# Kernel tuning notes

Hardware: AMD Instinct MI355X
Metric: run time of the kernel (lower is better)

The kernel has to match this reference:

```python
import jax, jax.numpy as jnp
import numpy as np

N, E = 50000, 800000
F_IN, C_PRE, C, G_HID = 16, 32, 64, 64
EPS = 1e-5


def graph_norm(x, batch, w, b, ms):
    # PyG GraphNorm over a single graph (batch all zeros)
    cnt = jax.ops.segment_sum(jnp.ones((x.shape[0], 1), x.dtype), batch, num_segments=1)
    mean = jax.ops.segment_sum(x, batch, num_segments=1) / cnt
    out = x - mean[batch] * ms
    var = jax.ops.segment_sum(out * out, batch, num_segments=1) / cnt
    std = jnp.sqrt(var + EPS)
    return w * out / std[batch] + b


def ggnn_conv(h, edge_index, edge_attr,
              gw1, gb1, gw2, gb2, gw3, gb3,
              zw, zb, rw, rb, hw, hb):
    n = h.shape[0]
    loops = jnp.arange(n)
    row = jnp.concatenate([edge_index[0], loops])  # sources (x_j)
    col = jnp.concatenate([edge_index[1], loops])  # targets (x_i), aggregation index
    ea = jnp.concatenate([edge_attr, jnp.ones((n, 1), h.dtype)], axis=0)
    deg = jax.ops.segment_sum(jnp.ones(col.shape[0], h.dtype), col, num_segments=n)
    dis = jnp.where(deg > 0, deg ** -0.5, 0.0)
    norm = dis[row] * dis[col]
    x_j = h[row]
    x_i = h[col]
    g = jnp.concatenate([x_i, x_j, ea], axis=-1)            # [E+N, 2C+1]
    g = jax.nn.relu(g @ gw1 + gb1)
    g = jax.nn.relu(g @ gw2 + gb2)
    gate = jax.nn.sigmoid(g @ gw3 + gb3)                     # [E+N, 1]
    msg = gate * (norm[:, None] * x_j)
    aggr = jax.ops.segment_sum(msg, col, num_segments=n)     # scatter-add
    zi = jnp.concatenate([h, aggr], axis=-1)
    z = jax.nn.sigmoid(zi @ zw + zb)
    r = jax.nn.sigmoid(zi @ rw + rb)
    hc = jax.nn.relu(jnp.concatenate([r * h, aggr], axis=-1) @ hw + hb)
    return (1.0 - z) * h + z * hc


def setup_inputs() -> dict:
    key = jax.random.key(0)
    ks = iter(jax.random.split(key, 40))

    def lin(k, fi, fo):
        return jax.random.normal(k, (fi, fo), jnp.float32) / np.sqrt(fi)

    inp = {
        'x': jax.random.normal(next(ks), (N, F_IN), jnp.float32),
        'edge_index': jax.random.randint(next(ks), (2, E), 0, N),
        'edge_attr': jax.random.uniform(next(ks), (E, 1), jnp.float32),
        'batch': jnp.zeros((N,), jnp.int32),
        'preproc_w': lin(next(ks), F_IN, C_PRE), 'preproc_b': jnp.zeros((C_PRE,), jnp.float32),
        'gn_pre_w': jnp.ones((C_PRE,), jnp.float32), 'gn_pre_b': jnp.zeros((C_PRE,), jnp.float32), 'gn_pre_ms': jnp.ones((C_PRE,), jnp.float32),
        'init_w': lin(next(ks), C_PRE, C), 'init_b': jnp.zeros((C,), jnp.float32),
        'gn_init_w': jnp.ones((C,), jnp.float32), 'gn_init_b': jnp.zeros((C,), jnp.float32), 'gn_init_ms': jnp.ones((C,), jnp.float32),
        'gate_w1': lin(next(ks), 2 * C + 1, G_HID), 'gate_b1': jnp.zeros((G_HID,), jnp.float32),
        'gate_w2': lin(next(ks), G_HID, G_HID), 'gate_b2': jnp.zeros((G_HID,), jnp.float32),
        'gate_w3': lin(next(ks), G_HID, 1), 'gate_b3': jnp.zeros((1,), jnp.float32),
        'lin_z_w': lin(next(ks), 2 * C, C), 'lin_z_b': jnp.zeros((C,), jnp.float32),
        'lin_r_w': lin(next(ks), 2 * C, C), 'lin_r_b': jnp.zeros((C,), jnp.float32),
        'lin_h_w': lin(next(ks), 2 * C, C), 'lin_h_b': jnp.zeros((C,), jnp.float32),
        'gn_ggnn_w': jnp.ones((C,), jnp.float32), 'gn_ggnn_b': jnp.zeros((C,), jnp.float32), 'gn_ggnn_ms': jnp.ones((C,), jnp.float32),
        'fc1_w': lin(next(ks), 2 * C, C), 'fc1_b': jnp.zeros((C,), jnp.float32),
        'gn_fc1_w': jnp.ones((C,), jnp.float32), 'gn_fc1_b': jnp.zeros((C,), jnp.float32), 'gn_fc1_ms': jnp.ones((C,), jnp.float32),
        'fc2_w': lin(next(ks), C, 2), 'fc2_b': jnp.zeros((2,), jnp.float32),
    }
    return inp


def reference(x, edge_index, edge_attr, batch,
              preproc_w, preproc_b, gn_pre_w, gn_pre_b, gn_pre_ms,
              init_w, init_b, gn_init_w, gn_init_b, gn_init_ms,
              gate_w1, gate_b1, gate_w2, gate_b2, gate_w3, gate_b3,
              lin_z_w, lin_z_b, lin_r_w, lin_r_b, lin_h_w, lin_h_b,
              gn_ggnn_w, gn_ggnn_b, gn_ggnn_ms,
              fc1_w, fc1_b, gn_fc1_w, gn_fc1_b, gn_fc1_ms,
              fc2_w, fc2_b):
    n_layers = 4
    h = x @ preproc_w + preproc_b
    h = graph_norm(h, batch, gn_pre_w, gn_pre_b, gn_pre_ms)
    h = jax.nn.relu(h)
    h0 = h @ init_w + init_b
    h0 = graph_norm(h0, batch, gn_init_w, gn_init_b, gn_init_ms)
    h0 = jax.nn.relu(h0)
    h = h0
    for _ in range(n_layers):  # tied GGNN layer
        h = ggnn_conv(h, edge_index, edge_attr,
                      gate_w1, gate_b1, gate_w2, gate_b2, gate_w3, gate_b3,
                      lin_z_w, lin_z_b, lin_r_w, lin_r_b, lin_h_w, lin_h_b)
        h = graph_norm(h, batch, gn_ggnn_w, gn_ggnn_b, gn_ggnn_ms)
    out = jnp.concatenate([h0, h], axis=1)
    out = out @ fc1_w + fc1_b
    out = graph_norm(out, batch, gn_fc1_w, gn_fc1_b, gn_fc1_ms)
    out = jax.nn.relu(out)
    out = out @ fc2_w + fc2_b  # [N, 2] logits
    return out
```

## Files before the change

kernel.cpp:

```cpp
#include <hip/hip_runtime.h>

#define GN_EPS 1e-5f

typedef _Float16 half8 __attribute__((ext_vector_type(8)));
typedef float floatx4 __attribute__((ext_vector_type(4)));

__device__ __forceinline__ float sigmoidf_(float x){ return 1.0f/(1.0f+__expf(-x)); }
__device__ __forceinline__ float bcast_(float v, int k){
  return __int_as_float(__builtin_amdgcn_readlane(__float_as_int(v), k));
}

__global__ void cnt_init_kernel(int* cnt, int n){
  int i = blockIdx.x*blockDim.x+threadIdx.x;
  if (i < n) cnt[i] = 1;
}
__global__ void cnt_kernel(const int* __restrict__ ei, int* cnt, int E){
  int e = blockIdx.x*blockDim.x+threadIdx.x;
  if (e < E) atomicAdd(&cnt[ei[E+e]], 1);
}
__global__ void dis_from_cnt_kernel(const int* __restrict__ cnt, float* dis, int n){
  int i = blockIdx.x*blockDim.x+threadIdx.x;
  if (i < n) dis[i] = rsqrtf((float)cnt[i]);
}
__global__ __launch_bounds__(256) void scan1_kernel(const int* __restrict__ cnt,
                                                    int* loc, int* bsum, int n){
  __shared__ int s[256];
  int t = threadIdx.x, i = blockIdx.x*256 + t;
  int v = (i < n) ? cnt[i] : 0;
  s[t] = v; __syncthreads();
  #pragma unroll
  for (int d = 1; d < 256; d <<= 1){
    int u = (t >= d) ? s[t-d] : 0; __syncthreads();
    s[t] += u; __syncthreads();
  }
  if (i < n) loc[i] = s[t] - v;
  if (t == 255) bsum[blockIdx.x] = s[255];
}
__global__ __launch_bounds__(256) void scan2_kernel(int* bsum, int nb){
  __shared__ int s[256];
  int t = threadIdx.x;
  int v = (t < nb) ? bsum[t] : 0;
  s[t] = v; __syncthreads();
  #pragma unroll
  for (int d = 1; d < 256; d <<= 1){
    int u = (t >= d) ? s[t-d] : 0; __syncthreads();
    s[t] += u; __syncthreads();
  }
  if (t < nb) bsum[t] = s[t] - v;
}
__global__ void scan3_kernel(const int* __restrict__ loc, const int* __restrict__ bsum,
                             int* rowptr, int n, int total){
  int i = blockIdx.x*blockDim.x+threadIdx.x;
  if (i < n) rowptr[i] = loc[i] + bsum[i >> 8];
  if (i == 0) rowptr[n] = total;
}
__global__ void scatter_kernel(const int* __restrict__ ei, const float* __restrict__ ea,
                               const int* __restrict__ rowptr, int* fill,
                               unsigned* sd, _Float16* ea2, int E, int n){
  int idx = blockIdx.x*blockDim.x+threadIdx.x;
  int tot = E + n;
  if (idx >= tot) return;
  int r, c; float v;
  if (idx < E){ r = ei[idx]; c = ei[E+idx]; v = ea[idx]; }
  else        { r = c = idx - E; v = 1.0f; }
  int j = rowptr[c] + atomicAdd(&fill[c], 1);
  sd[j] = (unsigned)r | ((unsigned)c << 16);
  ea2[j] = (_Float16)v;
}

__global__ __launch_bounds__(256) void wprep_kernel(
    const float* __restrict__ w1, const float* __restrict__ zw,
    const float* __restrict__ rw, const float* __restrict__ hw,
    const float* __restrict__ fw, const float* __restrict__ w2,
    _Float16* __restrict__ wp){
  int idx = blockIdx.x*256 + threadIdx.x;
  if (idx < 8192){
    int t=idx>>10, kh=(idx>>9)&1, g=(idx>>7)&3, l=(idx>>3)&15, j=idx&7;
    int kg=(t>=4?64:0)+kh*32+g*8+j;
    wp[idx] = (_Float16)w1[kg*64 + (t&3)*16 + l];
  } else if (idx < 40960){
    int m=(idx-8192)>>13, k=(idx-8192)&8191;
    int t=(k>>11)&3, kh=(k>>9)&3, g=(k>>7)&3, l=(k>>3)&15, j=k&7;
    const float* W = (m==0)?zw:((m==1)?rw:((m==2)?hw:fw));
    wp[idx] = (_Float16)W[(kh*32+g*8+j)*64 + t*16 + l];
  } else if (idx < 45056){
    int k = idx-40960;
    int t=(k>>10)&3, kh=(k>>9)&1, g=(k>>7)&3, l=(k>>3)&15, j=k&7;
    wp[idx] = (_Float16)w2[(kh*32+g*8+j)*64 + t*16 + l];
  }
}

template<int K_IN, int C_OUT>
__global__ __launch_bounds__(256) void mm1_kernel(
    const float* __restrict__ x, const float* __restrict__ W,
    const float* __restrict__ b, float* __restrict__ y, int n){
  __shared__ float sW[K_IN*C_OUT];
  for (int i = threadIdx.x; i < K_IN*C_OUT; i += 256) sW[i] = W[i];
  __syncthreads();
  const int lane = threadIdx.x & 63;
  const int col  = (lane < C_OUT) ? lane : 0;
  const float bias = b[col];
  int wid = (blockIdx.x*256 + threadIdx.x) >> 6;
  int nw  = (gridDim.x*256) >> 6;
  for (int i = wid; i < n; i += nw){
    float xv = (lane < K_IN) ? x[(size_t)i*K_IN + lane] : 0.0f;
    float a0 = bias, a1 = 0.0f;
    #pragma unroll
    for (int k = 0; k < K_IN; k += 2){
      a0 += bcast_(xv, k  ) * sW[(k  )*C_OUT + col];
      a1 += bcast_(xv, k+1) * sW[(k+1)*C_OUT + col];
    }
    if (lane < C_OUT) y[(size_t)i*C_OUT + lane] = a0 + a1;
  }
}

template<int RELU, int WRITE_H0>
__global__ __launch_bounds__(256) void normpq_kernel(
    const float* __restrict__ hin, float* __restrict__ hout,
    float* __restrict__ h0out,
    const float* __restrict__ stats,
    const float* __restrict__ gw, const float* __restrict__ gb,
    const float* __restrict__ gms,
    const _Float16* __restrict__ w1p, const float* __restrict__ b1,
    _Float16* __restrict__ Ph, _Float16* __restrict__ QH, int n)
{
  __shared__ _Float16 sB[8192];
  __shared__ float sSO[128];
  for (int i = threadIdx.x; i < 1024; i += 256)
    ((half8*)sB)[i] = ((const half8*)w1p)[i];
  if (threadIdx.x < 64){
    int ch = threadIdx.x;
    float invN = 1.0f/(float)n;
    float mean = stats[ch]*invN;
    float mm = mean*gms[ch];
    float var = stats[64+ch]*invN - mm*(2.0f*mean - mm);
    float inv = rsqrtf(fmaxf(var,0.f)+GN_EPS);
    float sc = inv*gw[ch];
    sSO[ch] = sc;
    sSO[64+ch] = gb[ch] - mm*sc;
  }
  __syncthreads();
  const int lane = threadIdx.x & 63;
  const int g16 = lane>>4, l16 = lane&15;
  float scA[8], ofA[8], scB[8], ofB[8];
  #pragma unroll
  for (int j = 0; j < 8; ++j){
    scA[j]=sSO[g16*8+j];    ofA[j]=sSO[64+g16*8+j];
    scB[j]=sSO[32+g16*8+j]; ofB[j]=sSO[96+g16*8+j];
  }
  float b1f[4];
  #pragma unroll
  for (int t = 0; t < 4; ++t) b1f[t] = b1[t*16 + l16];

  int wid = (blockIdx.x*blockDim.x + threadIdx.x) >> 6;
  int nw  = (gridDim.x*blockDim.x) >> 6;
  int tiles = (n + 15) >> 4;
  for (int tile = wid; tile < tiles; tile += nw){
    int base = tile*16;
    int na = min(base + l16, n-1);
    const float* hp = hin + (size_t)na*64;
    float4 a0 = *(const float4*)(hp + g16*8);
    float4 a1 = *(const float4*)(hp + g16*8 + 4);
    float4 c0 = *(const float4*)(hp + 32 + g16*8);
    float4 c1 = *(const float4*)(hp + 32 + g16*8 + 4);
    float va[8] = {a0.x,a0.y,a0.z,a0.w,a1.x,a1.y,a1.z,a1.w};
    float vb[8] = {c0.x,c0.y,c0.z,c0.w,c1.x,c1.y,c1.z,c1.w};
    half8 af0, af1;
    #pragma unroll
    for (int j = 0; j < 8; ++j){
      float v = va[j]*scA[j] + ofA[j];
      if (RELU) v = fmaxf(v, 0.f);
      va[j] = v; af0[j] = (_Float16)v;
      float u = vb[j]*scB[j] + ofB[j];
      if (RELU) u = fmaxf(u, 0.f);
      vb[j] = u; af1[j] = (_Float16)u;
    }
    float* op = hout + (size_t)na*64;
    *(float4*)(op + g16*8)       = (float4){va[0],va[1],va[2],va[3]};
    *(float4*)(op + g16*8 + 4)   = (float4){va[4],va[5],va[6],va[7]};
    *(float4*)(op + 32 + g16*8)  = (float4){vb[0],vb[1],vb[2],vb[3]};
    *(float4*)(op + 32 + g16*8+4)= (float4){vb[4],vb[5],vb[6],vb[7]};
    if (WRITE_H0){
      float* o2 = h0out + (size_t)na*64;
      *(float4*)(o2 + g16*8)       = (float4){va[0],va[1],va[2],va[3]};
      *(float4*)(o2 + g16*8 + 4)   = (float4){va[4],va[5],va[6],va[7]};
      *(float4*)(o2 + 32 + g16*8)  = (float4){vb[0],vb[1],vb[2],vb[3]};
      *(float4*)(o2 + 32 + g16*8+4)= (float4){vb[4],vb[5],vb[6],vb[7]};
    }
    *(half8*)(QH + (size_t)na*128 + 64 + g16*8) = af0;
    *(half8*)(QH + (size_t)na*128 + 96 + g16*8) = af1;

    floatx4 acc[8];
    #pragma unroll
    for (int t = 0; t < 8; ++t){
      float bv = (t < 4) ? b1f[t] : 0.0f;
      acc[t] = (floatx4){bv, bv, bv, bv};
    }
    #pragma unroll
    for (int t = 0; t < 8; ++t){
      half8 bf0 = *(const half8*)&sB[((t*2+0)*4+g16)*128 + l16*8];
      half8 bf1 = *(const half8*)&sB[((t*2+1)*4+g16)*128 + l16*8];
      acc[t] = __builtin_amdgcn_mfma_f32_16x16x32_f16(af0, bf0, acc[t], 0, 0, 0);
      acc[t] = __builtin_amdgcn_mfma_f32_16x16x32_f16(af1, bf1, acc[t], 0, 0, 0);
    }
    #pragma unroll
    for (int t = 0; t < 8; ++t)
      #pragma unroll
      for (int rg = 0; rg < 4; ++rg){
        int nd = base + g16*4 + rg;
        if (nd < n){
          if (t < 4) Ph[(size_t)nd*64  + t*16 + l16]      = (_Float16)acc[t][rg];
          else       QH[(size_t)nd*128 + (t-4)*16 + l16]  = (_Float16)acc[t][rg];
        }
      }
  }
}

__global__ __launch_bounds__(256) void gru_mfma_kernel(
    float* __restrict__ h, float* __restrict__ aggr,
    const float* __restrict__ dis, const _Float16* __restrict__ QH,
    const _Float16* __restrict__ gwp,
    const float* __restrict__ zb, const float* __restrict__ rb,
    const float* __restrict__ hb,
    float* __restrict__ stats, int n)
{
  __shared__ _Float16 sW[3*8192];
  __shared__ _Float16 sRH[4][16][72];
  __shared__ float sSt[128];
  if (threadIdx.x < 128) sSt[threadIdx.x] = 0.f;
  for (int i = threadIdx.x; i < 3072; i += 256)
    ((half8*)sW)[i] = ((const half8*)gwp)[i];
  __syncthreads();
  const int lane = threadIdx.x & 63;
  const int g16 = lane>>4, l16 = lane&15;
  const int w = threadIdx.x >> 6;
  float zbf[4], rbf[4], hbf[4];
  #pragma unroll
  for (int t = 0; t < 4; ++t){
    zbf[t] = zb[t*16+l16]; rbf[t] = rb[t*16+l16]; hbf[t] = hb[t*16+l16];
  }
  float ssum[4] = {0,0,0,0}, ssq[4] = {0,0,0,0};
#define GW(m,t,kh) (*(const half8*)&sW[(m)*8192 + (((t)*4+(kh))*4+g16)*128 + l16*8])

  int wid = (blockIdx.x*blockDim.x + threadIdx.x) >> 6;
  int nw  = (gridDim.x*blockDim.x) >> 6;
  int tiles = (n + 15) >> 4;
  for (int tile = wid; tile < tiles; tile += nw){
    int base = tile*16;
    int na = min(base + l16, n-1);
    float dv = dis[na];
    half8 af[4];
    af[0] = *(const half8*)(QH + (size_t)na*128 + 64 + g16*8);
    af[1] = *(const half8*)(QH + (size_t)na*128 + 96 + g16*8);
    #pragma unroll
    for (int kh = 0; kh < 2; ++kh){
      float* ar = aggr + (size_t)na*64 + kh*32 + g16*8;
      float4 a0 = *(const float4*)ar;
      float4 a1 = *(const float4*)(ar+4);
      *(float4*)(ar)   = (float4){0,0,0,0};
      *(float4*)(ar+4) = (float4){0,0,0,0};
      half8 t8;
      t8[0]=(_Float16)(a0.x*dv); t8[1]=(_Float16)(a0.y*dv);
      t8[2]=(_Float16)(a0.z*dv); t8[3]=(_Float16)(a0.w*dv);
      t8[4]=(_Float16)(a1.x*dv); t8[5]=(_Float16)(a1.y*dv);
      t8[6]=(_Float16)(a1.z*dv); t8[7]=(_Float16)(a1.w*dv);
      af[2+kh] = t8;
    }
    floatx4 az[4], ar4[4];
    #pragma unroll
    for (int t = 0; t < 4; ++t){
      az[t]  = (floatx4){zbf[t], zbf[t], zbf[t], zbf[t]};
      ar4[t] = (floatx4){rbf[t], rbf[t], rbf[t], rbf[t]};
      #pragma unroll
      for (int kh = 0; kh < 4; ++kh){
        az[t]  = __builtin_amdgcn_mfma_f32_16x16x32_f16(af[kh], GW(0,t,kh), az[t],  0, 0, 0);
        ar4[t] = __builtin_amdgcn_mfma_f32_16x16x32_f16(af[kh], GW(1,t,kh), ar4[t], 0, 0, 0);
      }
    }
    float zr[16], hv[16];
    #pragma unroll
    for (int t = 0; t < 4; ++t)
      #pragma unroll
      for (int rg = 0; rg < 4; ++rg){
        int ndc = min(base + g16*4 + rg, n-1);
        float hval = h[(size_t)ndc*64 + t*16 + l16];
        float zv = sigmoidf_(az[t][rg]);
        float rv = sigmoidf_(ar4[t][rg]);
        zr[t*4+rg] = zv; hv[t*4+rg] = hval;
        sRH[w][g16*4+rg][t*16+l16] = (_Float16)(rv*hval);
      }
    asm volatile("s_waitcnt lgkmcnt(0)" ::: "memory");
    __builtin_amdgcn_sched_barrier(0);
    half8 af2_0 = *(const half8*)&sRH[w][l16][g16*8];
    half8 af2_1 = *(const half8*)&sRH[w][l16][32 + g16*8];
    floatx4 ah[4];
    #pragma unroll
    for (int t = 0; t < 4; ++t){
      ah[t] = (floatx4){hbf[t], hbf[t], hbf[t], hbf[t]};
      ah[t] = __builtin_amdgcn_mfma_f32_16x16x32_f16(af2_0, GW(2,t,0), ah[t], 0, 0, 0);
      ah[t] = __builtin_amdgcn_mfma_f32_16x16x32_f16(af2_1, GW(2,t,1), ah[t], 0, 0, 0);
      ah[t] = __builtin_amdgcn_mfma_f32_16x16x32_f16(af[2],  GW(2,t,2), ah[t], 0, 0, 0);
      ah[t] = __builtin_amdgcn_mfma_f32_16x16x32_f16(af[3],  GW(2,t,3), ah[t], 0, 0, 0);
    }
    #pragma unroll
    for (int t = 0; t < 4; ++t)
      #pragma unroll
      for (int rg = 0; rg < 4; ++rg){
        int nd = base + g16*4 + rg;
        if (nd < n){
          float hc = fmaxf(ah[t][rg], 0.f);
          float zv = zr[t*4+rg];
          float hn = (1.f - zv)*hv[t*4+rg] + zv*hc;
          h[(size_t)nd*64 + t*16 + l16] = hn;
          ssum[t] += hn; ssq[t] += hn*hn;
        }
      }
  }
#undef GW
  #pragma unroll
  for (int t = 0; t < 4; ++t){
    atomicAdd(&sSt[t*16+l16], ssum[t]);
    atomicAdd(&sSt[64+t*16+l16], ssq[t]);
  }
  __syncthreads();
  if (threadIdx.x < 128) atomicAdd(&stats[threadIdx.x], sSt[threadIdx.x]);
}

__global__ __launch_bounds__(256) void fc1_mfma_kernel(
    const float* __restrict__ h0, const float* __restrict__ h,
    const _Float16* __restrict__ fp, const float* __restrict__ b,
    float* __restrict__ out, float* __restrict__ stats, int n)
{
  __shared__ _Float16 sB[8192];
  __shared__ float sSt[128];
  if (threadIdx.x < 128) sSt[threadIdx.x] = 0.f;
  for (int i = threadIdx.x; i < 1024; i += 256)
    ((half8*)sB)[i] = ((const half8*)fp)[i];
  __syncthreads();
  const int lane = threadIdx.x & 63;
  const int g16 = lane>>4, l16 = lane&15;
  float bf[4];
  #pragma unroll
  for (int t = 0; t < 4; ++t) bf[t] = b[t*16+l16];
  float ssum[4] = {0,0,0,0}, ssq[4] = {0,0,0,0};

  int wid = (blockIdx.x*blockDim.x + threadIdx.x) >> 6;
  int nw  = (gridDim.x*blockDim.x) >> 6;
  int tiles = (n + 15) >> 4;
  for (int tile = wid; tile < tiles; tile += nw){
    int base = tile*16;
    int na = min(base + l16, n-1);
    half8 af[4];
    #pragma unroll
    for (int kh = 0; kh < 4; ++kh){
      const float* sp = (kh < 2 ? h0 : h) + (size_t)na*64 + (kh&1)*32 + g16*8;
      float4 a0 = *(const float4*)sp;
      float4 a1 = *(const float4*)(sp+4);
      half8 t8;
      t8[0]=(_Float16)a0.x; t8[1]=(_Float16)a0.y; t8[2]=(_Float16)a0.z; t8[3]=(_Float16)a0.w;
      t8[4]=(_Float16)a1.x; t8[5]=(_Float16)a1.y; t8[6]=(_Float16)a1.z; t8[7]=(_Float16)a1.w;
      af[kh] = t8;
    }
    #pragma unroll
    for (int t = 0; t < 4; ++t){
      floatx4 acc = (floatx4){bf[t], bf[t], bf[t], bf[t]};
      #pragma unroll
      for (int kh = 0; kh < 4; ++kh)
        acc = __builtin_amdgcn_mfma_f32_16x16x32_f16(af[kh],
                *(const half8*)&sB[((t*4+kh)*4+g16)*128 + l16*8], acc, 0, 0, 0);
      #pragma unroll
      for (int rg = 0; rg < 4; ++rg){
        int nd = base + g16*4 + rg;
        if (nd < n){
          float v = acc[rg];
          out[(size_t)nd*64 + t*16 + l16] = v;
          ssum[t] += v; ssq[t] += v*v;
        }
      }
    }
  }
  #pragma unroll
  for (int t = 0; t < 4; ++t){
    atomicAdd(&sSt[t*16+l16], ssum[t]);
    atomicAdd(&sSt[64+t*16+l16], ssq[t]);
  }
  __syncthreads();
  if (threadIdx.x < 128) atomicAdd(&stats[threadIdx.x], sSt[threadIdx.x]);
}

__global__ __launch_bounds__(256) void edge_tile_kernel(
    const unsigned* __restrict__ sd, const _Float16* __restrict__ ea2,
    const _Float16* __restrict__ Ph, const _Float16* __restrict__ QH,
    const float* __restrict__ dis,
    const _Float16* __restrict__ w2p, const float* __restrict__ b2,
    const float* __restrict__ w1e, const float* __restrict__ w3,
    const float* __restrict__ b3,
    float* __restrict__ aggr, float* __restrict__ stats, int EN)
{
  if (blockIdx.x == 0 && threadIdx.x < 128) stats[threadIdx.x] = 0.f;

  const int lane = threadIdx.x & 63;
  const int g16  = lane >> 4;
  const int l16  = lane & 15;

  half8 bfrag[4][2];
  #pragma unroll
  for (int t = 0; t < 4; ++t)
    #pragma unroll
    for (int kh = 0; kh < 2; ++kh)
      bfrag[t][kh] = *(const half8*)&w2p[t*1024 + kh*512 + g16*128 + l16*8];

  half8 w1h[2];
  #pragma unroll
  for (int kh = 0; kh < 2; ++kh)
    #pragma unroll
    for (int j = 0; j < 8; ++j)
      w1h[kh][j] = (_Float16)w1e[kh*32 + g16*8 + j];

  float w3f[4], b2f[4];
  #pragma unroll
  for (int t = 0; t < 4; ++t){ w3f[t] = w3[t*16 + l16]; b2f[t] = b2[t*16 + l16]; }
  const float b3v = b3[0];
  const _Float16* QHh = QH + 64;

  int wid = (blockIdx.x*blockDim.x + threadIdx.x) >> 6;
  int nw  = (gridDim.x*blockDim.x) >> 6;
  int tiles = (EN + 15) >> 4;

  for (int tile = wid; tile < tiles; tile += nw){
    int e0 = tile << 4;
    int m = EN - e0; if (m > 16) m = 16;
    int el = e0 + ((l16 < m) ? l16 : (m-1));
    unsigned sdv = sd[el];
    int r = (int)(sdv & 0xffffu);
    int c = (int)(sdv >> 16);
    float dv = (l16 < m) ? dis[r] : 0.0f;
    _Float16 eavh = ea2[el];

    half8 hq0 = *(const half8*)(QH + (size_t)r*128 + g16*8);
    half8 hq1 = *(const half8*)(QH + (size_t)r*128 + 32 + g16*8);
    half8 p0  = *(const half8*)(Ph + (size_t)c*64 + g16*8);
    half8 p1  = *(const half8*)(Ph + (size_t)c*64 + 32 + g16*8);

    _Float16 hv16[16];
    #pragma unroll
    for (int i = 0; i < 16; ++i){
      int ri = __builtin_amdgcn_readlane(r, i);
      hv16[i] = QHh[(size_t)ri*128 + lane];
    }

    half8 e8;
    #pragma unroll
    for (int j = 0; j < 8; ++j) e8[j] = eavh;
    half8 a0h = p0 + hq0 + w1h[0]*e8;
    half8 a1h = p1 + hq1 + w1h[1]*e8;
    #pragma unroll
    for (int j = 0; j < 8; ++j){
      a0h[j] = a0h[j] > (_Float16)0.f ? a0h[j] : (_Float16)0.f;
      a1h[j] = a1h[j] > (_Float16)0.f ? a1h[j] : (_Float16)0.f;
    }

    floatx4 acc[4];
    #pragma unroll
    for (int t4 = 0; t4 < 4; ++t4)
      acc[t4] = (floatx4){b2f[t4], b2f[t4], b2f[t4], b2f[t4]};
    __builtin_amdgcn_s_setprio(1);
    #pragma unroll
    for (int t4 = 0; t4 < 4; ++t4){
      acc[t4] = __builtin_amdgcn_mfma_f32_16x16x32_f16(a0h, bfrag[t4][0], acc[t4], 0, 0, 0);
      acc[t4] = __builtin_amdgcn_mfma_f32_16x16x32_f16(a1h, bfrag[t4][1], acc[t4], 0, 0, 0);
    }
    __builtin_amdgcn_s_setprio(0);

    float s[4] = {0.f,0.f,0.f,0.f};
    #pragma unroll
    for (int t4 = 0; t4 < 4; ++t4)
      #pragma unroll
      for (int rg = 0; rg < 4; ++rg)
        s[rg] += fmaxf(acc[t4][rg], 0.0f) * w3f[t4];
    #pragma unroll
    for (int rg = 0; rg < 4; ++rg){
      #pragma unroll
      for (int off = 1; off < 16; off <<= 1)
        s[rg] += __shfl_xor(s[rg], off);
      s[rg] = sigmoidf_(s[rg] + b3v);
    }

    float fs[4];
    #pragma unroll
    for (int rg = 0; rg < 4; ++rg){
      float dvp = __shfl(dv, (g16 << 4) | (g16*4 + rg));
      fs[rg] = s[rg] * dvp;
    }

    int cnext = __shfl(c, (lane & 48) | ((l16 + 1) & 15));
    unsigned long long bm = __ballot(c != cnext);
    unsigned bmask = ((unsigned)bm | 0x8000u) & 0xffffu;

    float accv = 0.f;
    #pragma unroll
    for (int i = 0; i < 16; ++i){
      float gi = bcast_(fs[i & 3], (i >> 2) << 4);
      accv = fmaf(gi, (float)hv16[i], accv);
      if ((bmask >> i) & 1){
        int ci = __builtin_amdgcn_readlane(c, i);
        atomicAdd(&aggr[(size_t)ci*64 + lane], accv);
        accv = 0.f;
      }
    }
  }
}

template<int C>
__global__ __launch_bounds__(256) void norm_stats_kernel(
    const float* __restrict__ x, int n, float* __restrict__ stats){
  __shared__ float ssum[256], ssq[256];
  const int tid = threadIdx.x;
  const int c = tid % C;
  int row = (blockIdx.x*256 + tid) / C;
  int stride = (gridDim.x*256) / C;
  float s = 0.f, q = 0.f;
  for (int i = row; i < n; i += stride){
    float v = x[(size_t)i*C + c];
    s += v; q += v*v;
  }
  ssum[tid] = s; ssq[tid] = q;
  __syncthreads();
  if (tid < C){
    float S = 0.f, Q2 = 0.f;
    for (int t = tid; t < 256; t += C){ S += ssum[t]; Q2 += ssq[t]; }
    atomicAdd(&stats[tid], S);
    atomicAdd(&stats[C + tid], Q2);
  }
}

template<int C, int RELU>
__global__ __launch_bounds__(256) void norm_apply_kernel(
    const float* __restrict__ x, const float* __restrict__ stats,
    const float* __restrict__ w, const float* __restrict__ b,
    const float* __restrict__ ms, float* __restrict__ y, int n){
  const float invN = 1.0f / (float)n;
  size_t idx = blockIdx.x*256 + threadIdx.x;
  size_t step = (size_t)gridDim.x*256;
  size_t tot = (size_t)n*C;
  for (; idx < tot; idx += step){
    int c = idx % C;
    float mean = stats[c] * invN;
    float mm = mean * ms[c];
    float var = stats[C + c]*invN - mm*(2.0f*mean - mm);
    float inv = rsqrtf(fmaxf(var, 0.0f) + GN_EPS);
    float v = (x[idx] - mm)*inv*w[c] + b[c];
    if (RELU) v = fmaxf(v, 0.0f);
    y[idx] = v;
  }
}

__global__ void fc2_kernel(
    const float* __restrict__ x, const float* __restrict__ w,
    const float* __restrict__ b, float* __restrict__ out, int n){
  int i = blockIdx.x*blockDim.x + threadIdx.x;
  if (i >= n) return;
  float a0 = b[0], a1 = b[1];
  const float4* xr = (const float4*)(x + (size_t)i*64);
  #pragma unroll
  for (int k4 = 0; k4 < 16; ++k4){
    float4 v = xr[k4];
    int k = k4*4;
    a0 += v.x*w[(k+0)*2+0] + v.y*w[(k+1)*2+0] + v.z*w[(k+2)*2+0] + v.w*w[(k+3)*2+0];
    a1 += v.x*w[(k+0)*2+1] + v.y*w[(k+1)*2+1] + v.z*w[(k+2)*2+1] + v.w*w[(k+3)*2+1];
  }
  out[i*2+0] = a0;
  out[i*2+1] = a1;
}

extern "C" void kernel_launch(void* const* d_in, const int* in_sizes, int n_in,
                              void* d_out, int out_size, void* d_ws, size_t ws_size,
                              hipStream_t stream){
  const float* x          = (const float*)d_in[0];
  const int*   ei         = (const int*)  d_in[1];
  const float* ea         = (const float*)d_in[2];
  const float* preproc_w  = (const float*)d_in[4];
  const float* preproc_b  = (const float*)d_in[5];
  const float* gn_pre_w   = (const float*)d_in[6];
  const float* gn_pre_b   = (const float*)d_in[7];
  const float* gn_pre_ms  = (const float*)d_in[8];
  const float* init_w     = (const float*)d_in[9];
  const float* init_b     = (const float*)d_in[10];
  const float* gn_init_w  = (const float*)d_in[11];
  const float* gn_init_b  = (const float*)d_in[12];
  const float* gn_init_ms = (const float*)d_in[13];
  const float* gate_w1    = (const float*)d_in[14];
  const float* gate_b1    = (const float*)d_in[15];
  const float* gate_w2    = (const float*)d_in[16];
  const float* gate_b2    = (const float*)d_in[17];
  const float* gate_w3    = (const float*)d_in[18];
  const float* gate_b3    = (const float*)d_in[19];
  const float* lin_z_w    = (const float*)d_in[20];
  const float* lin_z_b    = (const float*)d_in[21];
  const float* lin_r_w    = (const float*)d_in[22];
  const float* lin_r_b    = (const float*)d_in[23];
  const float* lin_h_w    = (const float*)d_in[24];
  const float* lin_h_b    = (const float*)d_in[25];
  const float* gn_ggnn_w  = (const float*)d_in[26];
  const float* gn_ggnn_b  = (const float*)d_in[27];
  const float* gn_ggnn_ms = (const float*)d_in[28];
  const float* fc1_w      = (const float*)d_in[29];
  const float* fc1_b      = (const float*)d_in[30];
  const float* gn_fc1_w   = (const float*)d_in[31];
  const float* gn_fc1_b   = (const float*)d_in[32];
  const float* gn_fc1_ms  = (const float*)d_in[33];
  const float* fc2_w      = (const float*)d_in[34];
  const float* fc2_b      = (const float*)d_in[35];

  const int N = in_sizes[3];
  const int E = in_sizes[1] / 2;
  const int EN = E + N;

  float* base = (float*)d_ws;
  const size_t R = (size_t)64*N;
  float* h     = base;
  float* h0    = h    + R;
  float* Preg  = h0   + R;
  float* aggr  = Preg + R;
  float* QHreg = aggr + R;
  float* dis   = QHreg + R;
  float* stats = dis + N;
  size_t need = (5*R + N + 128) * sizeof(float);
  if (ws_size < need || N > 65535) return;

  _Float16* Ph  = (_Float16*)Preg;
  _Float16* QH  = (_Float16*)QHreg;
  unsigned* sd  = (unsigned*)(Preg + 32*(size_t)N);
  _Float16* ea2 = (_Float16*)(sd + EN);
  _Float16* wp  = (_Float16*)(((uintptr_t)(ea2 + EN) + 15) & ~(uintptr_t)15);
  _Float16* w1p = wp;
  _Float16* gwp = wp + 8192;
  _Float16* fc1p= wp + 32768;
  _Float16* w2p = wp + 40960;

  int* cnt    = (int*)aggr;
  int* loc    = cnt + N;
  int* fill   = loc + N;
  int* bsum   = fill + N;
  int* rowptr = bsum + 256;

  const int GB = 1024;
  const int RB = 784;
  const int EB = 3072;
  const int nb = (N + 255) / 256;

  cnt_init_kernel<<<(N+255)/256, 256, 0, stream>>>(cnt, N);
  cnt_kernel<<<(E+255)/256, 256, 0, stream>>>(ei, cnt, E);
  dis_from_cnt_kernel<<<(N+255)/256, 256, 0, stream>>>(cnt, dis, N);
  scan1_kernel<<<nb, 256, 0, stream>>>(cnt, loc, bsum, N);
  scan2_kernel<<<1, 256, 0, stream>>>(bsum, nb);
  scan3_kernel<<<nb, 256, 0, stream>>>(loc, bsum, rowptr, N, EN);
  hipMemsetAsync(fill, 0, (size_t)N*sizeof(int), stream);
  scatter_kernel<<<(EN+255)/256, 256, 0, stream>>>(ei, ea, rowptr, fill, sd, ea2, E, N);
  wprep_kernel<<<176, 256, 0, stream>>>(gate_w1, lin_z_w, lin_r_w, lin_h_w, fc1_w, gate_w2, wp);
  hipMemsetAsync(aggr, 0, R*sizeof(float), stream);

  mm1_kernel<16,32><<<GB, 256, 0, stream>>>(x, preproc_w, preproc_b, h0, N);
  hipMemsetAsync(stats, 0, 2*64*sizeof(float), stream);
  norm_stats_kernel<32><<<256, 256, 0, stream>>>(h0, N, stats);
  norm_apply_kernel<32,1><<<2048, 256, 0, stream>>>(h0, stats, gn_pre_w, gn_pre_b, gn_pre_ms, h, N);

  mm1_kernel<32,64><<<GB, 256, 0, stream>>>(h, init_w, init_b, h0, N);
  hipMemsetAsync(stats, 0, 2*64*sizeof(float), stream);
  norm_stats_kernel<64><<<256, 256, 0, stream>>>(h0, N, stats);
  normpq_kernel<1,1><<<RB, 256, 0, stream>>>(h0, h, h0, stats,
                                             gn_init_w, gn_init_b, gn_init_ms,
                                             w1p, gate_b1, Ph, QH, N);

  for (int layer = 0; layer < 4; ++layer){
    edge_tile_kernel<<<EB, 256, 0, stream>>>(sd, ea2, Ph, QH, dis,
                                             w2p, gate_b2, gate_w1 + 128*64,
                                             gate_w3, gate_b3, aggr, stats, EN);
    gru_mfma_kernel<<<RB, 256, 0, stream>>>(h, aggr, dis, QH, gwp,
                                            lin_z_b, lin_r_b, lin_h_b, stats, N);
    if (layer < 3)
      normpq_kernel<0,0><<<RB, 256, 0, stream>>>(h, h, nullptr, stats,
                                                 gn_ggnn_w, gn_ggnn_b, gn_ggnn_ms,
                                                 w1p, gate_b1, Ph, QH, N);
    else
      norm_apply_kernel<64,0><<<2048, 256, 0, stream>>>(h, stats, gn_ggnn_w, gn_ggnn_b, gn_ggnn_ms, h, N);
  }

  hipMemsetAsync(stats, 0, 2*64*sizeof(float), stream);
  fc1_mfma_kernel<<<RB, 256, 0, stream>>>(h0, h, fc1p, fc1_b, aggr, stats, N);
  norm_apply_kernel<64,1><<<2048, 256, 0, stream>>>(aggr, stats, gn_fc1_w, gn_fc1_b, gn_fc1_ms, h, N);

  fc2_kernel<<<(N+255)/256, 256, 0, stream>>>(h, fc2_w, fc2_b, (float*)d_out, N);
}
```

Baseline: 631.5 us.

## Fuse setup kernels, fold norm stats into mm1, move edge B-fragments to LDS

Merges the degree-count init, count and dis kernels into one count kernel plus a scan that also writes dis, and moves the fill reset into scan3. The GraphNorm statistics for the two preprocessing matmuls are now accumulated inside mm1_kernel, which drops the separate norm_stats passes. In the edge kernel, the W2 MFMA B-fragments are staged in shared memory and reloaded per tile instead of being held in registers. The aim is fewer launches, fewer re-reads of intermediate buffers, and lower register pressure, at the cost of extra LDS reads in the hot edge loop.

```diff
diff --git a/kernel.cpp b/kernel.cpp
--- a/kernel.cpp
+++ b/kernel.cpp
@@ -10,23 +10,18 @@
   return __int_as_float(__builtin_amdgcn_readlane(__float_as_int(v), k));
 }
 
-__global__ void cnt_init_kernel(int* cnt, int n){
+__global__ void cnt_all_kernel(const int* __restrict__ ei, int* cnt, int E, int n){
   int i = blockIdx.x*blockDim.x+threadIdx.x;
-  if (i < n) cnt[i] = 1;
-}
-__global__ void cnt_kernel(const int* __restrict__ ei, int* cnt, int E){
-  int e = blockIdx.x*blockDim.x+threadIdx.x;
-  if (e < E) atomicAdd(&cnt[ei[E+e]], 1);
-}
-__global__ void dis_from_cnt_kernel(const int* __restrict__ cnt, float* dis, int n){
-  int i = blockIdx.x*blockDim.x+threadIdx.x;
-  if (i < n) dis[i] = rsqrtf((float)cnt[i]);
+  if (i < n) atomicAdd(&cnt[i], 1);
+  if (i < E) atomicAdd(&cnt[ei[E+i]], 1);
 }
 __global__ __launch_bounds__(256) void scan1_kernel(const int* __restrict__ cnt,
-                                                    int* loc, int* bsum, int n){
+                                                    int* loc, int* bsum,
+                                                    float* __restrict__ dis, int n){
   __shared__ int s[256];
   int t = threadIdx.x, i = blockIdx.x*256 + t;
   int v = (i < n) ? cnt[i] : 0;
+  if (i < n) dis[i] = rsqrtf((float)v);
   s[t] = v; __syncthreads();
   #pragma unroll
   for (int d = 1; d < 256; d <<= 1){
@@ -49,9 +44,9 @@
   if (t < nb) bsum[t] = s[t] - v;
 }
 __global__ void scan3_kernel(const int* __restrict__ loc, const int* __restrict__ bsum,
-                             int* rowptr, int n, int total){
+                             int* rowptr, int* fill, int n, int total){
   int i = blockIdx.x*blockDim.x+threadIdx.x;
-  if (i < n) rowptr[i] = loc[i] + bsum[i >> 8];
+  if (i < n){ rowptr[i] = loc[i] + bsum[i >> 8]; fill[i] = 0; }
   if (i == 0) rowptr[n] = total;
 }
 __global__ void scatter_kernel(const int* __restrict__ ei, const float* __restrict__ ea,
@@ -90,11 +85,14 @@
   }
 }
 
-template<int K_IN, int C_OUT>
+template<int K_IN, int C_OUT, int STATS>
 __global__ __launch_bounds__(256) void mm1_kernel(
     const float* __restrict__ x, const float* __restrict__ W,
-    const float* __restrict__ b, float* __restrict__ y, int n){
+    const float* __restrict__ b, float* __restrict__ y,
+    float* __restrict__ stats, int n){
   __shared__ float sW[K_IN*C_OUT];
+  __shared__ float sSt[2*C_OUT];
+  if (STATS && threadIdx.x < 2*C_OUT) sSt[threadIdx.x] = 0.f;
   for (int i = threadIdx.x; i < K_IN*C_OUT; i += 256) sW[i] = W[i];
   __syncthreads();
   const int lane = threadIdx.x & 63;
@@ -102,6 +100,7 @@
   const float bias = b[col];
   int wid = (blockIdx.x*256 + threadIdx.x) >> 6;
   int nw  = (gridDim.x*256) >> 6;
+  float qs = 0.f, qq = 0.f;
   for (int i = wid; i < n; i += nw){
     float xv = (lane < K_IN) ? x[(size_t)i*K_IN + lane] : 0.0f;
     float a0 = bias, a1 = 0.0f;
@@ -110,7 +109,19 @@
       a0 += bcast_(xv, k  ) * sW[(k  )*C_OUT + col];
       a1 += bcast_(xv, k+1) * sW[(k+1)*C_OUT + col];
     }
-    if (lane < C_OUT) y[(size_t)i*C_OUT + lane] = a0 + a1;
+    if (lane < C_OUT){
+      float v = a0 + a1;
+      y[(size_t)i*C_OUT + lane] = v;
+      if (STATS){ qs += v; qq += v*v; }
+    }
+  }
+  if (STATS){
+    if (lane < C_OUT){
+      atomicAdd(&sSt[lane], qs);
+      atomicAdd(&sSt[C_OUT+lane], qq);
+    }
+    __syncthreads();
+    if (threadIdx.x < 2*C_OUT) atomicAdd(&stats[threadIdx.x], sSt[threadIdx.x]);
   }
 }
 
@@ -397,18 +408,15 @@
     const float* __restrict__ b3,
     float* __restrict__ aggr, float* __restrict__ stats, int EN)
 {
+  __shared__ _Float16 sB[4096];
   if (blockIdx.x == 0 && threadIdx.x < 128) stats[threadIdx.x] = 0.f;
+  for (int i = threadIdx.x; i < 512; i += 256)
+    ((half8*)sB)[i] = ((const half8*)w2p)[i];
+  __syncthreads();
 
   const int lane = threadIdx.x & 63;
   const int g16  = lane >> 4;
   const int l16  = lane & 15;
-
-  half8 bfrag[4][2];
-  #pragma unroll
-  for (int t = 0; t < 4; ++t)
-    #pragma unroll
-    for (int kh = 0; kh < 2; ++kh)
-      bfrag[t][kh] = *(const half8*)&w2p[t*1024 + kh*512 + g16*128 + l16*8];
 
   half8 w1h[2];
   #pragma unroll
@@ -467,8 +475,10 @@
     __builtin_amdgcn_s_setprio(1);
     #pragma unroll
     for (int t4 = 0; t4 < 4; ++t4){
-      acc[t4] = __builtin_amdgcn_mfma_f32_16x16x32_f16(a0h, bfrag[t4][0], acc[t4], 0, 0, 0);
-      acc[t4] = __builtin_amdgcn_mfma_f32_16x16x32_f16(a1h, bfrag[t4][1], acc[t4], 0, 0, 0);
+      half8 bf0 = *(const half8*)&sB[t4*1024 + g16*128 + l16*8];
+      half8 bf1 = *(const half8*)&sB[t4*1024 + 512 + g16*128 + l16*8];
+      acc[t4] = __builtin_amdgcn_mfma_f32_16x16x32_f16(a0h, bf0, acc[t4], 0, 0, 0);
+      acc[t4] = __builtin_amdgcn_mfma_f32_16x16x32_f16(a1h, bf1, acc[t4], 0, 0, 0);
     }
     __builtin_amdgcn_s_setprio(0);
 
@@ -508,29 +518,6 @@
         accv = 0.f;
       }
     }
-  }
-}
-
-template<int C>
-__global__ __launch_bounds__(256) void norm_stats_kernel(
-    const float* __restrict__ x, int n, float* __restrict__ stats){
-  __shared__ float ssum[256], ssq[256];
-  const int tid = threadIdx.x;
-  const int c = tid % C;
-  int row = (blockIdx.x*256 + tid) / C;
-  int stride = (gridDim.x*256) / C;
-  float s = 0.f, q = 0.f;
-  for (int i = row; i < n; i += stride){
-    float v = x[(size_t)i*C + c];
-    s += v; q += v*v;
-  }
-  ssum[tid] = s; ssq[tid] = q;
-  __syncthreads();
-  if (tid < C){
-    float S = 0.f, Q2 = 0.f;
-    for (int t = tid; t < 256; t += C){ S += ssum[t]; Q2 += ssq[t]; }
-    atomicAdd(&stats[tid], S);
-    atomicAdd(&stats[C + tid], Q2);
   }
 }
 
@@ -648,26 +635,23 @@
   const int RB = 784;
   const int EB = 3072;
   const int nb = (N + 255) / 256;
-
-  cnt_init_kernel<<<(N+255)/256, 256, 0, stream>>>(cnt, N);
-  cnt_kernel<<<(E+255)/256, 256, 0, stream>>>(ei, cnt, E);
-  dis_from_cnt_kernel<<<(N+255)/256, 256, 0, stream>>>(cnt, dis, N);
-  scan1_kernel<<<nb, 256, 0, stream>>>(cnt, loc, bsum, N);
+  const int mNE = (E > N ? E : N);
+
+  hipMemsetAsync(cnt, 0, (size_t)N*sizeof(int), stream);
+  cnt_all_kernel<<<(mNE+255)/256, 256, 0, stream>>>(ei, cnt, E, N);
+  scan1_kernel<<<nb, 256, 0, stream>>>(cnt, loc, bsum, dis, N);
   scan2_kernel<<<1, 256, 0, stream>>>(bsum, nb);
-  scan3_kernel<<<nb, 256, 0, stream>>>(loc, bsum, rowptr, N, EN);
-  hipMemsetAsync(fill, 0, (size_t)N*sizeof(int), stream);
+  scan3_kernel<<<nb, 256, 0, stream>>>(loc, bsum, rowptr, fill, N, EN);
   scatter_kernel<<<(EN+255)/256, 256, 0, stream>>>(ei, ea, rowptr, fill, sd, ea2, E, N);
   wprep_kernel<<<176, 256, 0, stream>>>(gate_w1, lin_z_w, lin_r_w, lin_h_w, fc1_w, gate_w2, wp);
   hipMemsetAsync(aggr, 0, R*sizeof(float), stream);
 
-  mm1_kernel<16,32><<<GB, 256, 0, stream>>>(x, preproc_w, preproc_b, h0, N);
   hipMemsetAsync(stats, 0, 2*64*sizeof(float), stream);
-  norm_stats_kernel<32><<<256, 256, 0, stream>>>(h0, N, stats);
+  mm1_kernel<16,32,1><<<GB, 256, 0, stream>>>(x, preproc_w, preproc_b, h0, stats, N);
   norm_apply_kernel<32,1><<<2048, 256, 0, stream>>>(h0, stats, gn_pre_w, gn_pre_b, gn_pre_ms, h, N);
 
-  mm1_kernel<32,64><<<GB, 256, 0, stream>>>(h, init_w, init_b, h0, N);
   hipMemsetAsync(stats, 0, 2*64*sizeof(float), stream);
-  norm_stats_kernel<64><<<256, 256, 0, stream>>>(h0, N, stats);
+  mm1_kernel<32,64,1><<<GB, 256, 0, stream>>>(h, init_w, init_b, h0, stats, N);
   normpq_kernel<1,1><<<RB, 256, 0, stream>>>(h0, h, h0, stats,
                                              gn_init_w, gn_init_b, gn_init_ms,
                                              w1p, gate_b1, Ph, QH, N);
```

Result: slower. 645.8 us (+2.3%).
